# Optimization experiments

Hardware: AMD Instinct MI355X
Metric: run time of the kernel (lower is better)

The kernel has to match this reference:

```python
import jax, jax.numpy as jnp
import numpy as np

EMBED_DIM = 768
NUM_HEADS = 12
HEAD_DIM = EMBED_DIM // NUM_HEADS


def setup_inputs() -> dict:
    key = jax.random.key(0)
    ks = jax.random.split(key, 9)
    B, N, D = 8, 1024, EMBED_DIM
    s = 1.0 / np.sqrt(D)
    x = jax.random.normal(ks[0], (B, N, D), dtype=jnp.float32)
    Wq = jax.random.normal(ks[1], (D, D), dtype=jnp.float32) * s
    bq = jnp.zeros((D,), dtype=jnp.float32)
    Wk = jax.random.normal(ks[2], (D, D), dtype=jnp.float32) * s
    bk = jnp.zeros((D,), dtype=jnp.float32)
    Wv = jax.random.normal(ks[3], (D, D), dtype=jnp.float32) * s
    bv = jnp.zeros((D,), dtype=jnp.float32)
    Wo = jax.random.normal(ks[4], (D, D), dtype=jnp.float32) * s
    bo = jnp.zeros((D,), dtype=jnp.float32)
    return {"x": x, "Wq": Wq, "bq": bq, "Wk": Wk, "bk": bk,
            "Wv": Wv, "bv": bv, "Wo": Wo, "bo": bo}


def reference(x, Wq, bq, Wk, bk, Wv, bv, Wo, bo):
    B, N, D = x.shape
    H, Hd = NUM_HEADS, HEAD_DIM
    # torch Linear: y = x @ W.T + b
    q = (x @ Wq.T + bq).reshape(B, N, H, Hd).transpose(0, 2, 1, 3)  # [B,H,N,Hd]
    k = (x @ Wk.T + bk).reshape(B, N, H, Hd).transpose(0, 2, 1, 3)
    v = (x @ Wv.T + bv).reshape(B, N, H, Hd).transpose(0, 2, 1, 3)
    # NOTE: original scales by embed_dim**-0.5 (not head_dim)
    scale = jnp.asarray(D, x.dtype) ** -0.5
    scores = jnp.einsum('bhnd,bhmd->bhnm', q, k) * scale  # [B,H,N,N]
    attn = jax.nn.softmax(scores, axis=-1)
    out = jnp.einsum('bhnm,bhmd->bhnd', attn, v)  # dropout: identity in eval
    out = out.transpose(0, 2, 1, 3).reshape(B, N, D)
    return out @ Wo.T + bo
```

## Files before the change

kernel.cpp:

```cpp
#include <hip/hip_runtime.h>
#include <math.h>


typedef __bf16 bf16x8 __attribute__((ext_vector_type(8)));
typedef float  f32x4  __attribute__((ext_vector_type(4)));
typedef unsigned u32x2 __attribute__((ext_vector_type(2)));
typedef unsigned u32x4 __attribute__((ext_vector_type(4)));
typedef unsigned short ushort_t;

__device__ __forceinline__ unsigned short f2bf(float f) {
    unsigned u = __float_as_uint(f);
    u += 0x7fffu + ((u >> 16) & 1u);
    return (unsigned short)(u >> 16);
}
__device__ __forceinline__ unsigned pk16(unsigned short lo, unsigned short hi) {
    return (unsigned)lo | ((unsigned)hi << 16);
}

#define GLL16(g, l)                                                                        \
    __builtin_amdgcn_global_load_lds((const __attribute__((address_space(1))) void*)(g),   \
                                     (__attribute__((address_space(3))) void*)(l), 16, 0, 0)

__global__ __launch_bounds__(256)
void cast_all(const float* __restrict__ x,
              const float* __restrict__ w0, const float* __restrict__ w1,
              const float* __restrict__ w2, const float* __restrict__ w3,
              ushort_t* __restrict__ xb, ushort_t* __restrict__ wb0,
              ushort_t* __restrict__ wb1, ushort_t* __restrict__ wb2,
              ushort_t* __restrict__ wb3)
{
    const int y = blockIdx.y;
    if (y == 0) {
        const int i = (blockIdx.x * 256 + threadIdx.x) * 8;
        const float4 f0 = *(const float4*)(x + i);
        const float4 f1 = *(const float4*)(x + i + 4);
        ushort4 p0, p1;
        p0.x = f2bf(f0.x); p0.y = f2bf(f0.y); p0.z = f2bf(f0.z); p0.w = f2bf(f0.w);
        p1.x = f2bf(f1.x); p1.y = f2bf(f1.y); p1.z = f2bf(f1.z); p1.w = f2bf(f1.w);
        *(ushort4*)(xb + i)     = p0;
        *(ushort4*)(xb + i + 4) = p1;
        return;
    }
    const int tile = blockIdx.x * 4 + (threadIdx.x >> 6);
    if (tile >= 48 * 24) return;
    const float* s; ushort_t* d;
    switch (y) {
        case 1:  s = w0; d = wb0; break;
        case 2:  s = w1; d = wb1; break;
        case 3:  s = w2; d = wb2; break;
        default: s = w3; d = wb3; break;
    }
    const int t = tile / 24, kb = tile % 24;
    const int L = threadIdx.x & 63, c = L & 15, g = L >> 4;
    const float* sp = s + (size_t)(t * 16 + c) * 768 + kb * 32 + g * 8;
    const float4 f0 = *(const float4*)sp;
    const float4 f1 = *(const float4*)(sp + 4);
    ushort4 p0, p1;
    p0.x = f2bf(f0.x); p0.y = f2bf(f0.y); p0.z = f2bf(f0.z); p0.w = f2bf(f0.w);
    p1.x = f2bf(f1.x); p1.y = f2bf(f1.y); p1.z = f2bf(f1.z); p1.w = f2bf(f1.w);
    ushort_t* dp = d + ((size_t)tile * 64 + L) * 8;
    *(ushort4*)dp       = p0;
    *(ushort4*)(dp + 4) = p1;
}

__global__ __launch_bounds__(256, 3)
void gemm_qkv(const ushort_t* __restrict__ xb,
              const ushort_t* __restrict__ wqb, const ushort_t* __restrict__ wkb,
              const ushort_t* __restrict__ wvb,
              const float* __restrict__ bq, const float* __restrict__ bk,
              const float* __restrict__ bv,
              ushort_t* __restrict__ Qh, ushort_t* __restrict__ Kl,
              ushort_t* __restrict__ Vl)
{
    __shared__ ushort_t smem[9216];
    ushort_t* As = smem;

    const int tid = threadIdx.x, L = tid & 63, wv = tid >> 6;
    const int c = L & 15, g = L >> 4;
    const int n0 = blockIdx.x * 128, m0 = blockIdx.y * 64;

    const int qs = ((tid & 3) ^ ((tid >> 3) & 3)) * 8;
    const ushort_t* ap = xb + (size_t)(m0 + (tid >> 2)) * 768 + qs;
    const int sg = (g ^ ((c >> 1) & 3)) * 8;

    const size_t wbase = ((size_t)(blockIdx.x * 8 + wv * 2) * 24 * 64 + L) * 8;
    const ushort_t* wqp = wqb + wbase;
    const ushort_t* wkp = wkb + wbase;
    const ushort_t* wvp = wvb + wbase;

    f32x4 acc[3][4][2];
#pragma unroll
    for (int z = 0; z < 3; ++z)
#pragma unroll
        for (int i = 0; i < 4; ++i)
#pragma unroll
            for (int j = 0; j < 2; ++j) acc[z][i][j] = (f32x4){0.f, 0.f, 0.f, 0.f};

    bf16x8 wf[3][2];
#pragma unroll
    for (int j = 0; j < 2; ++j) {
        wf[0][j] = *(const bf16x8*)(wqp + j * 12288);
        wf[1][j] = *(const bf16x8*)(wkp + j * 12288);
        wf[2][j] = *(const bf16x8*)(wvp + j * 12288);
    }

    GLL16(ap, &As[(size_t)tid * 8]);

    for (int kb = 0; kb < 24; ++kb) {
        __syncthreads();
        if (kb < 23)
            GLL16(ap + (kb + 1) * 32,
                  &As[((kb + 1) & 1) * 2048 + (size_t)tid * 8]);
        const ushort_t* Ab = &As[(kb & 1) * 2048];
        bf16x8 af[4];
#pragma unroll
        for (int i = 0; i < 4; ++i)
            af[i] = *(const bf16x8*)&Ab[(i * 16 + c) * 32 + sg];
#pragma unroll
        for (int z = 0; z < 3; ++z)
#pragma unroll
            for (int i = 0; i < 4; ++i)
#pragma unroll
                for (int j = 0; j < 2; ++j)
                    acc[z][i][j] = __builtin_amdgcn_mfma_f32_16x16x32_bf16(
                        af[i], wf[z][j], acc[z][i][j], 0, 0, 0);
        const int kn = (kb < 23) ? kb + 1 : 23;
#pragma unroll
        for (int j = 0; j < 2; ++j) {
            wf[0][j] = *(const bf16x8*)(wqp + j * 12288 + kn * 512);
            wf[1][j] = *(const bf16x8*)(wkp + j * 12288 + kn * 512);
            wf[2][j] = *(const bf16x8*)(wvp + j * 12288 + kn * 512);
        }
    }

    const int b  = m0 >> 10, nb = m0 & 1023;
    const int hcol = n0 + wv * 32;
    const int h = hcol >> 6, uh = (hcol >> 5) & 1;
    const int bh = b * 12 + h;
    ushort_t* scr = smem + wv * 2304;

    float bias2[3][2];
#pragma unroll
    for (int j = 0; j < 2; ++j) {
        bias2[0][j] = bq[hcol + j * 16 + c];
        bias2[1][j] = bk[hcol + j * 16 + c];
        bias2[2][j] = bv[hcol + j * 16 + c];
    }

    __syncthreads();

#pragma unroll
    for (int i = 0; i < 4; ++i)
#pragma unroll
        for (int j = 0; j < 2; ++j)
#pragma unroll
            for (int r = 0; r < 4; ++r)
                scr[(i * 16 + g * 4 + r) * 36 + j * 16 + c] =
                    f2bf(acc[0][i][j][r] + bias2[0][j]);
#pragma unroll
    for (int e = 0; e < 4; ++e) {
        const int slot = e * 64 + L;
        const int row = slot >> 2, ch = slot & 3;
        const u32x4 v = *(const u32x4*)&scr[row * 36 + ch * 8];
        *(u32x4*)&Qh[((size_t)bh * 1024 + nb + row) * 64 + uh * 32 + ch * 8] = v;
    }

#pragma unroll
    for (int i = 0; i < 4; ++i)
#pragma unroll
        for (int j = 0; j < 2; ++j)
#pragma unroll
            for (int r = 0; r < 4; ++r)
                scr[(i * 16 + g * 4 + r) * 36 + j * 16 + c] =
                    f2bf(acc[1][i][j][r] + bias2[1][j]);
#pragma unroll
    for (int tau = 0; tau < 4; ++tau) {
        const u32x4 v = *(const u32x4*)&scr[(tau * 16 + c) * 36 + g * 8];
        *(u32x4*)&Kl[(((size_t)bh * 64 + (nb >> 4) + tau) * 2 + uh) * 512
                     + (size_t)L * 8] = v;
    }

#pragma unroll
    for (int i = 0; i < 4; ++i)
#pragma unroll
        for (int j = 0; j < 2; ++j)
#pragma unroll
            for (int r = 0; r < 4; ++r)
                scr[(j * 16 + c) * 68 + i * 16 + g * 4 + r] =
                    f2bf(acc[2][i][j][r] + bias2[2][j]);
    const int T = nb >> 6;
#pragma unroll
    for (int t = 0; t < 4; ++t) {
        const int htl = t >> 1, u = t & 1;
        const u32x4 v = *(const u32x4*)&scr[(htl * 16 + c) * 68 + u * 32 + g * 8];
        *(u32x4*)&Vl[((((size_t)bh * 4 + uh * 2 + htl) * 16 + T) * 2 + u) * 512
                     + (size_t)L * 8] = v;
    }
}

__global__ __launch_bounds__(256, 3)
void gemm_outp(const ushort_t* __restrict__ attnb, const ushort_t* __restrict__ wob,
               const float* __restrict__ bo, float* __restrict__ out)
{
    __shared__ ushort_t smem[4096];
    ushort_t* As = smem;
    const int tid = threadIdx.x, L = tid & 63, wv = tid >> 6;
    const int c = L & 15, g = L >> 4;
    const int n0 = blockIdx.x * 128, m0 = blockIdx.y * 64;
    const int qs = ((tid & 3) ^ ((tid >> 3) & 3)) * 8;
    const ushort_t* ap = attnb + (size_t)(m0 + (tid >> 2)) * 768 + qs;
    const int sg = (g ^ ((c >> 1) & 3)) * 8;

    const size_t wbase = ((size_t)(blockIdx.x * 8 + wv * 2) * 24 * 64 + L) * 8;
    const ushort_t* wop = wob + wbase;

    f32x4 acc[4][2];
#pragma unroll
    for (int i = 0; i < 4; ++i)
#pragma unroll
        for (int j = 0; j < 2; ++j) acc[i][j] = (f32x4){0.f, 0.f, 0.f, 0.f};

    bf16x8 wf[2];
#pragma unroll
    for (int j = 0; j < 2; ++j) wf[j] = *(const bf16x8*)(wop + j * 12288);

    GLL16(ap, &As[(size_t)tid * 8]);

    for (int kb = 0; kb < 24; ++kb) {
        __syncthreads();
        if (kb < 23)
            GLL16(ap + (kb + 1) * 32,
                  &As[((kb + 1) & 1) * 2048 + (size_t)tid * 8]);
        const ushort_t* Ab = &As[(kb & 1) * 2048];
        bf16x8 af[4];
#pragma unroll
        for (int i = 0; i < 4; ++i)
            af[i] = *(const bf16x8*)&Ab[(i * 16 + c) * 32 + sg];
#pragma unroll
        for (int i = 0; i < 4; ++i)
#pragma unroll
            for (int j = 0; j < 2; ++j)
                acc[i][j] = __builtin_amdgcn_mfma_f32_16x16x32_bf16(
                    af[i], wf[j], acc[i][j], 0, 0, 0);
        const int kn = (kb < 23) ? kb + 1 : 23;
#pragma unroll
        for (int j = 0; j < 2; ++j)
            wf[j] = *(const bf16x8*)(wop + j * 12288 + kn * 512);
    }

#pragma unroll
    for (int i = 0; i < 4; ++i) {
        const int row = m0 + i * 16 + g * 4;
#pragma unroll
        for (int j = 0; j < 2; ++j) {
            const int col = n0 + wv * 32 + j * 16 + c;
            const float bsvo = bo[col];
#pragma unroll
            for (int r = 0; r < 4; ++r)
                out[(size_t)(row + r) * 768 + col] = acc[i][j][r] + bsvo;
        }
    }
}

__global__ __launch_bounds__(64, 3)
void flash_bf16(const ushort_t* __restrict__ Q, const ushort_t* __restrict__ Kl,
                const ushort_t* __restrict__ Vl, ushort_t* __restrict__ attnb)
{
    __shared__ ushort_t Ps[2][2][16 * 68];
    const int L = threadIdx.x;
    const int c = L & 15, g = L >> 4;
    const int bh = blockIdx.x, q0 = blockIdx.y * 32;
    const float SC2 = 0.05205954985329743f;

    const ushort_t* Qp = Q + ((size_t)bh * 1024 + q0 + c) * 64 + g * 8;
    bf16x8 qf[2][2];
    qf[0][0] = *(const bf16x8*)Qp;
    qf[0][1] = *(const bf16x8*)(Qp + 32);
    qf[1][0] = *(const bf16x8*)(Qp + 16 * 64);
    qf[1][1] = *(const bf16x8*)(Qp + 16 * 64 + 32);

    const ushort_t* Kb = Kl + (size_t)bh * 65536 + (size_t)L * 8;
    const ushort_t* Vb = Vl + (size_t)bh * 65536 + (size_t)L * 8;

    f32x4 o[2][4];
#pragma unroll
    for (int w = 0; w < 2; ++w)
#pragma unroll
        for (int ht = 0; ht < 4; ++ht) o[w][ht] = (f32x4){0.f, 0.f, 0.f, 0.f};
    float ls[2] = {0.f, 0.f};

    bf16x8 kf0[4], kf1[4];
#pragma unroll
    for (int ct = 0; ct < 4; ++ct) {
        kf0[ct] = *(const bf16x8*)(Kb + (size_t)(ct * 2 + 0) * 512);
        kf1[ct] = *(const bf16x8*)(Kb + (size_t)(ct * 2 + 1) * 512);
    }

    for (int T0 = 0; T0 < 16; T0 += 2) {
#pragma unroll
        for (int p = 0; p < 2; ++p) {
            const int T = T0 + p;
            bf16x8 vf0[4], vf1[4];
#pragma unroll
            for (int ht = 0; ht < 4; ++ht) {
                const ushort_t* vp = Vb + (size_t)((ht * 16 + T) * 2) * 512;
                vf0[ht] = *(const bf16x8*)vp;
                vf1[ht] = *(const bf16x8*)(vp + 512);
            }
            f32x4 s[2][4];
#pragma unroll
            for (int w = 0; w < 2; ++w)
#pragma unroll
                for (int ct = 0; ct < 4; ++ct) {
                    f32x4 zz = (f32x4){0.f, 0.f, 0.f, 0.f};
                    zz = __builtin_amdgcn_mfma_f32_16x16x32_bf16(kf0[ct], qf[w][0], zz, 0, 0, 0);
                    zz = __builtin_amdgcn_mfma_f32_16x16x32_bf16(kf1[ct], qf[w][1], zz, 0, 0, 0);
                    s[w][ct] = zz;
                }
            const int Tn = (T < 15) ? T + 1 : 15;
#pragma unroll
            for (int ct = 0; ct < 4; ++ct) {
                const ushort_t* kp = Kb + (size_t)((Tn * 4 + ct) * 2) * 512;
                kf0[ct] = *(const bf16x8*)kp;
                kf1[ct] = *(const bf16x8*)(kp + 512);
            }
#pragma unroll
            for (int w = 0; w < 2; ++w) {
#pragma unroll
                for (int ct = 0; ct < 4; ++ct) {
                    float pv[4];
#pragma unroll
                    for (int r = 0; r < 4; ++r)
                        pv[r] = __builtin_amdgcn_exp2f(s[w][ct][r] * SC2);
                    ls[w] += (pv[0] + pv[1]) + (pv[2] + pv[3]);
                    const unsigned w01 = __builtin_amdgcn_perm(
                        __float_as_uint(pv[1]), __float_as_uint(pv[0]), 0x07060302u);
                    const unsigned w23 = __builtin_amdgcn_perm(
                        __float_as_uint(pv[3]), __float_as_uint(pv[2]), 0x07060302u);
                    *(u32x2*)&Ps[p][w][c * 68 + ct * 16 + g * 4] = (u32x2){w01, w23};
                }
            }
#pragma unroll
            for (int w = 0; w < 2; ++w) {
                const int pb = c * 68 + g * 8;
                const u32x4 pa  = *(const u32x4*)&Ps[p][w][pb];
                const u32x4 pbv = *(const u32x4*)&Ps[p][w][pb + 32];
                const bf16x8 pf0 = __builtin_bit_cast(bf16x8, pa);
                const bf16x8 pf1 = __builtin_bit_cast(bf16x8, pbv);
#pragma unroll
                for (int ht = 0; ht < 4; ++ht) {
                    o[w][ht] = __builtin_amdgcn_mfma_f32_16x16x32_bf16(vf0[ht], pf0, o[w][ht], 0, 0, 0);
                    o[w][ht] = __builtin_amdgcn_mfma_f32_16x16x32_bf16(vf1[ht], pf1, o[w][ht], 0, 0, 0);
                }
            }
        }
    }

    const int b = bh / 12, h = bh % 12;
#pragma unroll
    for (int w = 0; w < 2; ++w) {
        float l = ls[w];
        l += __shfl_xor(l, 16);
        l += __shfl_xor(l, 32);
        const float inv = 1.f / l;
#pragma unroll
        for (int ht = 0; ht < 4; ++ht) {
            const unsigned w0 = pk16(f2bf(o[w][ht][0] * inv), f2bf(o[w][ht][1] * inv));
            const unsigned w1 = pk16(f2bf(o[w][ht][2] * inv), f2bf(o[w][ht][3] * inv));
            *(u32x2*)&Ps[0][w][c * 68 + ht * 16 + g * 4] = (u32x2){w0, w1};
        }
#pragma unroll
        for (int e = 0; e < 2; ++e) {
            const int row = e * 8 + (L >> 3);
            const int ch  = L & 7;
            const int si  = row * 68 + ch * 8;
            const u32x2 t0 = *(const u32x2*)&Ps[0][w][si];
            const u32x2 t1 = *(const u32x2*)&Ps[0][w][si + 4];
            *(u32x4*)&attnb[((size_t)(b * 1024 + q0 + w * 16 + row)) * 768 + h * 64 + ch * 8]
                = (u32x4){t0.x, t0.y, t1.x, t1.y};
        }
    }
}

extern "C" void kernel_launch(void* const* d_in, const int* in_sizes, int n_in,
                              void* d_out, int out_size, void* d_ws, size_t ws_size,
                              hipStream_t stream)
{
    const float* x  = (const float*)d_in[0];
    const float* Wq = (const float*)d_in[1];
    const float* bq = (const float*)d_in[2];
    const float* Wk = (const float*)d_in[3];
    const float* bk = (const float*)d_in[4];
    const float* Wv = (const float*)d_in[5];
    const float* bv = (const float*)d_in[6];
    const float* Wo = (const float*)d_in[7];
    const float* bo = (const float*)d_in[8];
    float* out = (float*)d_out;

    char* ws = (char*)d_ws;
    ushort_t* xb    = (ushort_t*)(ws);
    ushort_t* wqb   = (ushort_t*)(ws + 12582912);
    ushort_t* wkb   = (ushort_t*)(ws + 12582912 + 1179648);
    ushort_t* wvb   = (ushort_t*)(ws + 12582912 + 2359296);
    ushort_t* wob   = (ushort_t*)(ws + 12582912 + 3538944);
    ushort_t* Qh    = (ushort_t*)(ws + 17301504);
    ushort_t* Kl    = (ushort_t*)(ws + 29884416);
    ushort_t* Vl    = (ushort_t*)(ws + 42467328);
    ushort_t* attnb = (ushort_t*)(ws + 55050240);

    cast_all<<<dim3(3072, 5), 256, 0, stream>>>(x, Wq, Wk, Wv, Wo,
                                                xb, wqb, wkb, wvb, wob);
    gemm_qkv<<<dim3(6, 128), 256, 0, stream>>>(xb, wqb, wkb, wvb,
                                               bq, bk, bv, Qh, Kl, Vl);
    flash_bf16<<<dim3(96, 32), 64, 0, stream>>>(Qh, Kl, Vl, attnb);
    gemm_outp<<<dim3(6, 128), 256, 0, stream>>>(attnb, wob, bo, out);
}
```

Measured before the change: 187.7 us.

## Compact cast grid, relax GEMM waitcnt barriers, add MFMA priority hints in flash

The cast kernel's 2D grid, which launched mostly empty blocks for the four weight casts, becomes a compact 1D grid of exactly the needed blocks. In both GEMMs, the A-tile async load is issued before the weight register loads, and __syncthreads is replaced by an explicit s_waitcnt with a nonzero vmcnt plus s_barrier. This lets the weight prefetches stay in flight across the barrier instead of draining all memory ops. The flash kernel wraps its MFMA sections in s_setprio to favour matrix issue across waves. The vmcnt counts rely on exact instruction ordering, so a miscount risks reading LDS before the async copy lands.

```diff
diff --git a/kernel.cpp b/kernel.cpp
--- a/kernel.cpp
+++ b/kernel.cpp
@@ -29,9 +29,9 @@
               ushort_t* __restrict__ wb1, ushort_t* __restrict__ wb2,
               ushort_t* __restrict__ wb3)
 {
-    const int y = blockIdx.y;
-    if (y == 0) {
-        const int i = (blockIdx.x * 256 + threadIdx.x) * 8;
+    const int bid = blockIdx.x;
+    if (bid < 3072) {
+        const int i = (bid * 256 + threadIdx.x) * 8;
         const float4 f0 = *(const float4*)(x + i);
         const float4 f1 = *(const float4*)(x + i + 4);
         ushort4 p0, p1;
@@ -41,13 +41,13 @@
         *(ushort4*)(xb + i + 4) = p1;
         return;
     }
-    const int tile = blockIdx.x * 4 + (threadIdx.x >> 6);
-    if (tile >= 48 * 24) return;
+    const int wt = (bid - 3072) * 4 + (threadIdx.x >> 6);
+    const int wsel = wt / 1152, tile = wt % 1152;
     const float* s; ushort_t* d;
-    switch (y) {
-        case 1:  s = w0; d = wb0; break;
-        case 2:  s = w1; d = wb1; break;
-        case 3:  s = w2; d = wb2; break;
+    switch (wsel) {
+        case 0:  s = w0; d = wb0; break;
+        case 1:  s = w1; d = wb1; break;
+        case 2:  s = w2; d = wb2; break;
         default: s = w3; d = wb3; break;
     }
     const int t = tile / 24, kb = tile % 24;
@@ -96,6 +96,9 @@
 #pragma unroll
             for (int j = 0; j < 2; ++j) acc[z][i][j] = (f32x4){0.f, 0.f, 0.f, 0.f};
 
+    GLL16(ap, &As[(size_t)tid * 8]);
+    __builtin_amdgcn_sched_barrier(0);
+
     bf16x8 wf[3][2];
 #pragma unroll
     for (int j = 0; j < 2; ++j) {
@@ -104,13 +107,15 @@
         wf[2][j] = *(const bf16x8*)(wvp + j * 12288);
     }
 
-    GLL16(ap, &As[(size_t)tid * 8]);
-
     for (int kb = 0; kb < 24; ++kb) {
-        __syncthreads();
-        if (kb < 23)
+        asm volatile("s_waitcnt vmcnt(6) lgkmcnt(0)" ::: "memory");
+        __builtin_amdgcn_s_barrier();
+        __builtin_amdgcn_sched_barrier(0);
+        if (kb < 23) {
             GLL16(ap + (kb + 1) * 32,
                   &As[((kb + 1) & 1) * 2048 + (size_t)tid * 8]);
+            __builtin_amdgcn_sched_barrier(0);
+        }
         const ushort_t* Ab = &As[(kb & 1) * 2048];
         bf16x8 af[4];
 #pragma unroll
@@ -220,17 +225,22 @@
 #pragma unroll
         for (int j = 0; j < 2; ++j) acc[i][j] = (f32x4){0.f, 0.f, 0.f, 0.f};
 
+    GLL16(ap, &As[(size_t)tid * 8]);
+    __builtin_amdgcn_sched_barrier(0);
+
     bf16x8 wf[2];
 #pragma unroll
     for (int j = 0; j < 2; ++j) wf[j] = *(const bf16x8*)(wop + j * 12288);
 
-    GLL16(ap, &As[(size_t)tid * 8]);
-
     for (int kb = 0; kb < 24; ++kb) {
-        __syncthreads();
-        if (kb < 23)
+        asm volatile("s_waitcnt vmcnt(2) lgkmcnt(0)" ::: "memory");
+        __builtin_amdgcn_s_barrier();
+        __builtin_amdgcn_sched_barrier(0);
+        if (kb < 23) {
             GLL16(ap + (kb + 1) * 32,
                   &As[((kb + 1) & 1) * 2048 + (size_t)tid * 8]);
+            __builtin_amdgcn_sched_barrier(0);
+        }
         const ushort_t* Ab = &As[(kb & 1) * 2048];
         bf16x8 af[4];
 #pragma unroll
@@ -308,6 +318,7 @@
                 vf1[ht] = *(const bf16x8*)(vp + 512);
             }
             f32x4 s[2][4];
+            __builtin_amdgcn_s_setprio(1);
 #pragma unroll
             for (int w = 0; w < 2; ++w)
 #pragma unroll
@@ -317,6 +328,7 @@
                     zz = __builtin_amdgcn_mfma_f32_16x16x32_bf16(kf1[ct], qf[w][1], zz, 0, 0, 0);
                     s[w][ct] = zz;
                 }
+            __builtin_amdgcn_s_setprio(0);
             const int Tn = (T < 15) ? T + 1 : 15;
 #pragma unroll
             for (int ct = 0; ct < 4; ++ct) {
@@ -340,6 +352,7 @@
                     *(u32x2*)&Ps[p][w][c * 68 + ct * 16 + g * 4] = (u32x2){w01, w23};
                 }
             }
+            __builtin_amdgcn_s_setprio(1);
 #pragma unroll
             for (int w = 0; w < 2; ++w) {
                 const int pb = c * 68 + g * 8;
@@ -353,6 +366,7 @@
                     o[w][ht] = __builtin_amdgcn_mfma_f32_16x16x32_bf16(vf1[ht], pf1, o[w][ht], 0, 0, 0);
                 }
             }
+            __builtin_amdgcn_s_setprio(0);
         }
     }
 
@@ -408,8 +422,8 @@
     ushort_t* Vl    = (ushort_t*)(ws + 42467328);
     ushort_t* attnb = (ushort_t*)(ws + 55050240);
 
-    cast_all<<<dim3(3072, 5), 256, 0, stream>>>(x, Wq, Wk, Wv, Wo,
-                                                xb, wqb, wkb, wvb, wob);
+    cast_all<<<dim3(4224), 256, 0, stream>>>(x, Wq, Wk, Wv, Wo,
+                                             xb, wqb, wkb, wvb, wob);
     gemm_qkv<<<dim3(6, 128), 256, 0, stream>>>(xb, wqb, wkb, wvb,
                                                bq, bk, bv, Qh, Kl, Vl);
     flash_bf16<<<dim3(96, 32), 64, 0, stream>>>(Qh, Kl, Vl, attnb);
```

New measurement: 214.1 us. 1.14x slower.
